# Kernel optimization log

Hardware: AMD Instinct MI355X
Metric: run time of the kernel (lower is better)

The kernel has to match this reference:

```python
import jax, jax.numpy as jnp
import numpy as np

B, D = 128, 64  # batch; channel == height == width == dim == 64 (hardcoded by the module)


def setup_inputs() -> dict:
    key = jax.random.key(0)
    kx, kc, kh, kw = jax.random.split(key, 4)
    x = jax.random.normal(kx, (B, D, D, D), dtype=jnp.float32)
    # Stacked 1x1 conv weights: [i (loop index), out_channels, in_channels]
    Wc = jax.random.normal(kc, (D, D, D), dtype=jnp.float32) * 0.1
    Wh = jax.random.normal(kh, (D, D, D), dtype=jnp.float32) * 0.1
    Ww = jax.random.normal(kw, (D, D, D), dtype=jnp.float32) * 0.1
    return {"x": x, "Wc": Wc, "Wh": Wh, "Ww": Ww}


def reference(x, Wc, Wh, Ww):
    # x: [b, c, h, w] with c == h == w == 64
    # Adaptive avg-pool to 1x1 on three permutations -> three [b, 64] vectors.
    c_vec = x.mean(axis=(2, 3))  # pool over (h, w): channel descriptor   [b, 64]
    h_vec = x.mean(axis=(1, 2))  # pool over (c, h): width descriptor    [b, 64]
    w_vec = x.mean(axis=(1, 3))  # pool over (c, w): height descriptor   [b, 64]

    # All 64 per-iteration 1x1 convs + sigmoid as one batched GEMM per branch.
    # Wc[i, o, j]: weight of the i-th conv; conv(C)[o] = sum_j Wc[i,o,j] * c_vec[b,j]
    fc = jax.nn.sigmoid(jnp.einsum('ioj,bj->bio', Wc, c_vec))  # [b, 64(i), 64]
    fh = jax.nn.sigmoid(jnp.einsum('ioj,bj->bio', Wh, h_vec))  # [b, 64(i), 64]
    fw = jax.nn.sigmoid(jnp.einsum('ioj,bj->bio', Ww, w_vec))  # [b, 64(i), 64]

    # recon: bmm(bmm(C, H), W) == outer product fc_i (x) fh_i (x) fw_i, summed over i.
    LR = jnp.einsum('bic,bip,biq->bcpq', fc, fh, fw)  # [b, 64, 64, 64]
    return LR
```

## Files before the change

### kernel.cpp

```cpp
#include <hip/hip_runtime.h>
#include <hip/hip_bf16.h>


#define NB 128

typedef __attribute__((ext_vector_type(8))) short bf16x8;
typedef __attribute__((ext_vector_type(4))) float f32x4;

__device__ __forceinline__ float bf2f(short s) {
    return __uint_as_float(((unsigned)(unsigned short)s) << 16);
}
__device__ __forceinline__ unsigned packbf2(float a, float b) {
    unsigned ua = __float_as_uint(a); ua += 0x7fffu + ((ua >> 16) & 1u);
    unsigned ub = __float_as_uint(b); ub += 0x7fffu + ((ub >> 16) & 1u);
    return (ua >> 16) | (ub & 0xffff0000u);
}
__device__ __forceinline__ unsigned short f2bf(float f) {
    unsigned u = __float_as_uint(f); u += 0x7fffu + ((u >> 16) & 1u);
    return (unsigned short)(u >> 16);
}

__global__ __launch_bounds__(256) void pool_kernel(const float* __restrict__ x,
                                                   float* __restrict__ cvecT,
                                                   float* __restrict__ hv_part,
                                                   float* __restrict__ wv_part)
{
    const int blk  = blockIdx.x;
    const int b    = blk >> 2;
    const int cblk = blk & 3;
    const int t    = threadIdx.x;
    const int wv   = t >> 6;
    const int l    = t & 63;
    const int lg   = l >> 4;
    const int lw   = l & 15;

    __shared__ float cpart[16][4];
    __shared__ float hsum_l[64];
    __shared__ float wpart[4][64];

    const float* xb = x + (size_t)b * 262144 + (size_t)cblk * 65536;

    float cs[16];
    float acc_h[4] = {0.f, 0.f, 0.f, 0.f};
    float acc_w[4] = {0.f, 0.f, 0.f, 0.f};

#pragma unroll
    for (int cc = 0; cc < 16; ++cc) {
        const float* xc = xb + cc * 4096 + wv * 1024 + 4 * l;
        float sc = 0.f;
#pragma unroll
        for (int k = 0; k < 4; ++k) {
            float4 v = *reinterpret_cast<const float4*>(xc + k * 256);
            float s = (v.x + v.y) + (v.z + v.w);
            sc += s;
            acc_h[k] += s;
            acc_w[0] += v.x; acc_w[1] += v.y; acc_w[2] += v.z; acc_w[3] += v.w;
        }
        cs[cc] = sc;
    }

#pragma unroll
    for (int cc = 0; cc < 16; ++cc) {
        float v = cs[cc];
#pragma unroll
        for (int off = 32; off >= 1; off >>= 1) v += __shfl_xor(v, off, 64);
        if (l == 0) cpart[cc][wv] = v;
    }
#pragma unroll
    for (int k = 0; k < 4; ++k) {
        float v = acc_h[k];
        v += __shfl_xor(v, 1, 64);
        v += __shfl_xor(v, 2, 64);
        v += __shfl_xor(v, 4, 64);
        v += __shfl_xor(v, 8, 64);
        if (lw == 0) hsum_l[wv * 16 + k * 4 + lg] = v;
    }
#pragma unroll
    for (int m = 0; m < 4; ++m) {
        float v = acc_w[m];
        v += __shfl_xor(v, 16, 64);
        v += __shfl_xor(v, 32, 64);
        if (lg == 0) wpart[wv][lw * 4 + m] = v;
    }
    __syncthreads();

    const float scale = 1.f / 4096.f;
    if (t < 16) {
        float s = cpart[t][0] + cpart[t][1] + cpart[t][2] + cpart[t][3];
        cvecT[(cblk * 16 + t) * NB + b] = s * scale;
    }
    if (t < 64) {
        wv_part[(cblk * 64 + t) * NB + b] = hsum_l[t] * scale;
        float ws_ = wpart[0][t] + wpart[1][t] + wpart[2][t] + wpart[3][t];
        hv_part[(cblk * 64 + t) * NB + b] = ws_ * scale;
    }
}

__global__ __launch_bounds__(256) void fvec_kernel(const float* __restrict__ Wc,
                                                   const float* __restrict__ Wh,
                                                   const float* __restrict__ Ww,
                                                   const float* __restrict__ cvecT,
                                                   const float* __restrict__ hv_part,
                                                   const float* __restrict__ wv_part,
                                                   unsigned short* __restrict__ fcT,
                                                   unsigned short* __restrict__ fhT,
                                                   unsigned short* __restrict__ fwT)
{
    const int br = blockIdx.x >> 6;
    const int i  = blockIdx.x & 63;
    const float* W = (br == 0) ? Wc : (br == 1) ? Wh : Ww;
    const float* V = (br == 0) ? cvecT : (br == 1) ? hv_part : wv_part;
    unsigned short* outT = (br == 0) ? fcT : (br == 1) ? fhT : fwT;

    __shared__ float Wt[64][64];
    __shared__ float vl[64 * NB];

    const int t = threadIdx.x;
    {
        const float* Wi = W + (size_t)i * 4096;
#pragma unroll
        for (int r = 0; r < 4; ++r) {
            int f = t + 256 * r;
            float4 v = reinterpret_cast<const float4*>(Wi)[f];
            int o = (4 * f) >> 6;
            int j = (4 * f) & 63;
            Wt[j + 0][o] = v.x; Wt[j + 1][o] = v.y; Wt[j + 2][o] = v.z; Wt[j + 3][o] = v.w;
        }
    }
#pragma unroll
    for (int r = 0; r < 8; ++r) {
        int f = t + 256 * r;
        float4 v = reinterpret_cast<const float4*>(V)[f];
        if (br != 0) {
            float4 v1 = reinterpret_cast<const float4*>(V + 8192)[f];
            float4 v2 = reinterpret_cast<const float4*>(V + 16384)[f];
            float4 v3 = reinterpret_cast<const float4*>(V + 24576)[f];
            v.x += (v1.x + v2.x) + v3.x;
            v.y += (v1.y + v2.y) + v3.y;
            v.z += (v1.z + v2.z) + v3.z;
            v.w += (v1.w + v2.w) + v3.w;
        }
        reinterpret_cast<float4*>(vl)[f] = v;
    }
    __syncthreads();

    const int og = t & 7;
    const int bg = t >> 3;
    const int o0 = og * 8;
    const int b0 = bg * 4;

    float acc[4][8];
#pragma unroll
    for (int bb = 0; bb < 4; ++bb)
#pragma unroll
        for (int oo = 0; oo < 8; ++oo) acc[bb][oo] = 0.f;

#pragma unroll 4
    for (int j = 0; j < 64; ++j) {
        float4 vb = *reinterpret_cast<const float4*>(&vl[j * NB + b0]);
        float4 w0 = *reinterpret_cast<const float4*>(&Wt[j][o0]);
        float4 w1 = *reinterpret_cast<const float4*>(&Wt[j][o0 + 4]);
        float vb_[4] = {vb.x, vb.y, vb.z, vb.w};
        float wv_[8] = {w0.x, w0.y, w0.z, w0.w, w1.x, w1.y, w1.z, w1.w};
#pragma unroll
        for (int bb = 0; bb < 4; ++bb)
#pragma unroll
            for (int oo = 0; oo < 8; ++oo)
                acc[bb][oo] += vb_[bb] * wv_[oo];
    }

#pragma unroll
    for (int bb = 0; bb < 4; ++bb)
#pragma unroll
        for (int oo = 0; oo < 8; ++oo) {
            float sg = 1.f / (1.f + __expf(-acc[bb][oo]));
            outT[((size_t)(b0 + bb) * 64 + (o0 + oo)) * 64 + i] = f2bf(sg);
        }
}

__global__ __launch_bounds__(256) void recon_kernel(const unsigned short* __restrict__ fcT,
                                                    const unsigned short* __restrict__ fhT,
                                                    const unsigned short* __restrict__ fwT,
                                                    float* __restrict__ out)
{
    const int blk  = blockIdx.x;
    const int b    = blk >> 2;
    const int pblk = blk & 3;
    const int t    = threadIdx.x;
    const int w    = t >> 6;
    const int l    = t & 63;
    const int lr   = l & 15;
    const int lg4  = l >> 4;

    __shared__ __align__(16) unsigned short fcl[64 * 72];
    __shared__ __align__(16) unsigned short fwl[64 * 72];
    __shared__ __align__(16) unsigned short fhl[16 * 72];

    const unsigned short* fcb = fcT + (size_t)b * 4096;
    const unsigned short* fwb = fwT + (size_t)b * 4096;
    const unsigned short* fhb = fhT + (size_t)b * 4096 + pblk * 1024;

#pragma unroll
    for (int r = 0; r < 2; ++r) {
        int f = t + 256 * r;
        *reinterpret_cast<int4*>(&fcl[(f >> 3) * 72 + (f & 7) * 8]) =
            reinterpret_cast<const int4*>(fcb)[f];
        *reinterpret_cast<int4*>(&fwl[(f >> 3) * 72 + (f & 7) * 8]) =
            reinterpret_cast<const int4*>(fwb)[f];
    }
    if (t < 128) {
        *reinterpret_cast<int4*>(&fhl[(t >> 3) * 72 + (t & 7) * 8]) =
            reinterpret_cast<const int4*>(fhb)[t];
    }
    __syncthreads();

    bf16x8 afr[4][2], wfr[4][2];
#pragma unroll
    for (int ct = 0; ct < 4; ++ct)
#pragma unroll
        for (int kb = 0; kb < 2; ++kb) {
            afr[ct][kb] = *reinterpret_cast<const bf16x8*>(
                &fcl[(ct * 16 + lr) * 72 + kb * 32 + lg4 * 8]);
            wfr[ct][kb] = *reinterpret_cast<const bf16x8*>(
                &fwl[(ct * 16 + lr) * 72 + kb * 32 + lg4 * 8]);
        }

    for (int pp = 0; pp < 4; ++pp) {
        const int p = w * 4 + pp;
        float hv[16];
#pragma unroll
        for (int kb = 0; kb < 2; ++kb) {
            bf16x8 hf = *reinterpret_cast<const bf16x8*>(
                &fhl[p * 72 + kb * 32 + lg4 * 8]);
#pragma unroll
            for (int j = 0; j < 8; ++j) hv[kb * 8 + j] = bf2f(hf[j]);
        }
#pragma unroll
        for (int qt = 0; qt < 4; ++qt) {
            bf16x8 bfr0, bfr1;
            {
                union { unsigned u[4]; bf16x8 v; } bu;
#pragma unroll
                for (int jj = 0; jj < 4; ++jj) {
                    float p0 = hv[2 * jj]     * bf2f(wfr[qt][0][2 * jj]);
                    float p1 = hv[2 * jj + 1] * bf2f(wfr[qt][0][2 * jj + 1]);
                    bu.u[jj] = packbf2(p0, p1);
                }
                bfr0 = bu.v;
            }
            {
                union { unsigned u[4]; bf16x8 v; } bu;
#pragma unroll
                for (int jj = 0; jj < 4; ++jj) {
                    float p0 = hv[8 + 2 * jj]     * bf2f(wfr[qt][1][2 * jj]);
                    float p1 = hv[8 + 2 * jj + 1] * bf2f(wfr[qt][1][2 * jj + 1]);
                    bu.u[jj] = packbf2(p0, p1);
                }
                bfr1 = bu.v;
            }
#pragma unroll
            for (int ct = 0; ct < 4; ++ct) {
                f32x4 acc = {0.f, 0.f, 0.f, 0.f};
                acc = __builtin_amdgcn_mfma_f32_16x16x32_bf16(afr[ct][0], bfr0, acc, 0, 0, 0);
                acc = __builtin_amdgcn_mfma_f32_16x16x32_bf16(afr[ct][1], bfr1, acc, 0, 0, 0);
                float* ob = out + (((size_t)b * 64 + ct * 16 + lg4 * 4) * 64
                                   + (pblk * 16 + p)) * 64 + qt * 16 + lr;
#pragma unroll
                for (int r = 0; r < 4; ++r) ob[(size_t)r * 4096] = acc[r];
            }
        }
    }
}

extern "C" void kernel_launch(void* const* d_in, const int* in_sizes, int n_in,
                              void* d_out, int out_size, void* d_ws, size_t ws_size,
                              hipStream_t stream) {
    (void)in_sizes; (void)n_in; (void)out_size; (void)ws_size;
    const float* x  = (const float*)d_in[0];
    const float* Wc = (const float*)d_in[1];
    const float* Wh = (const float*)d_in[2];
    const float* Ww = (const float*)d_in[3];
    float* out = (float*)d_out;

    float* ws      = (float*)d_ws;
    float* cvecT   = ws;
    float* hv_part = ws + 8192;
    float* wv_part = ws + 40960;
    unsigned short* fcT = (unsigned short*)(ws + 73728);
    unsigned short* fhT = fcT + 524288;
    unsigned short* fwT = fhT + 524288;

    pool_kernel<<<512, 256, 0, stream>>>(x, cvecT, hv_part, wv_part);
    fvec_kernel<<<192, 256, 0, stream>>>(Wc, Wh, Ww, cvecT, hv_part, wv_part, fcT, fhT, fwT);
    recon_kernel<<<512, 256, 0, stream>>>(fcT, fhT, fwT, out);
}
```

Baseline: 77.66 us.

## Stage recon output through LDS for float4 stores; split pool across 8 blocks

The recon kernel now computes all four q-tiles per channel tile, writes the MFMA accumulators into a per-wave XOR-swizzled LDS bounce buffer, and reads them back as float4 rows. Each row is then stored contiguously, replacing the scattered 4-byte global stores and reducing store transactions on the 128 MB output. Separately, the pooling kernel is split into 8 channel blocks per batch instead of 4, doubling grid parallelism. This costs more partial sums for fvec_kernel to reduce and extra LDS usage in recon.

Result: faster. 70.86 us (-8.8%).

```diff
diff --git a/kernel.cpp b/kernel.cpp
--- a/kernel.cpp
+++ b/kernel.cpp
@@ -26,26 +26,26 @@
                                                    float* __restrict__ wv_part)
 {
     const int blk  = blockIdx.x;
-    const int b    = blk >> 2;
-    const int cblk = blk & 3;
+    const int b    = blk >> 3;
+    const int cblk = blk & 7;
     const int t    = threadIdx.x;
     const int wv   = t >> 6;
     const int l    = t & 63;
     const int lg   = l >> 4;
     const int lw   = l & 15;
 
-    __shared__ float cpart[16][4];
+    __shared__ float cpart[8][4];
     __shared__ float hsum_l[64];
     __shared__ float wpart[4][64];
 
-    const float* xb = x + (size_t)b * 262144 + (size_t)cblk * 65536;
-
-    float cs[16];
+    const float* xb = x + (size_t)b * 262144 + (size_t)cblk * 32768;
+
+    float cs[8];
     float acc_h[4] = {0.f, 0.f, 0.f, 0.f};
     float acc_w[4] = {0.f, 0.f, 0.f, 0.f};
 
 #pragma unroll
-    for (int cc = 0; cc < 16; ++cc) {
+    for (int cc = 0; cc < 8; ++cc) {
         const float* xc = xb + cc * 4096 + wv * 1024 + 4 * l;
         float sc = 0.f;
 #pragma unroll
@@ -60,7 +60,7 @@
     }
 
 #pragma unroll
-    for (int cc = 0; cc < 16; ++cc) {
+    for (int cc = 0; cc < 8; ++cc) {
         float v = cs[cc];
 #pragma unroll
         for (int off = 32; off >= 1; off >>= 1) v += __shfl_xor(v, off, 64);
@@ -85,9 +85,9 @@
     __syncthreads();
 
     const float scale = 1.f / 4096.f;
-    if (t < 16) {
+    if (t < 8) {
         float s = cpart[t][0] + cpart[t][1] + cpart[t][2] + cpart[t][3];
-        cvecT[(cblk * 16 + t) * NB + b] = s * scale;
+        cvecT[(cblk * 8 + t) * NB + b] = s * scale;
     }
     if (t < 64) {
         wv_part[(cblk * 64 + t) * NB + b] = hsum_l[t] * scale;
@@ -132,13 +132,11 @@
         int f = t + 256 * r;
         float4 v = reinterpret_cast<const float4*>(V)[f];
         if (br != 0) {
-            float4 v1 = reinterpret_cast<const float4*>(V + 8192)[f];
-            float4 v2 = reinterpret_cast<const float4*>(V + 16384)[f];
-            float4 v3 = reinterpret_cast<const float4*>(V + 24576)[f];
-            v.x += (v1.x + v2.x) + v3.x;
-            v.y += (v1.y + v2.y) + v3.y;
-            v.z += (v1.z + v2.z) + v3.z;
-            v.w += (v1.w + v2.w) + v3.w;
+#pragma unroll
+            for (int k = 1; k < 8; ++k) {
+                float4 u = reinterpret_cast<const float4*>(V + 8192 * k)[f];
+                v.x += u.x; v.y += u.y; v.z += u.z; v.w += u.w;
+            }
         }
         reinterpret_cast<float4*>(vl)[f] = v;
     }
@@ -195,6 +193,7 @@
     __shared__ __align__(16) unsigned short fcl[64 * 72];
     __shared__ __align__(16) unsigned short fwl[64 * 72];
     __shared__ __align__(16) unsigned short fhl[16 * 72];
+    __shared__ __align__(16) float bounce[4][16 * 72];
 
     const unsigned short* fcb = fcT + (size_t)b * 4096;
     const unsigned short* fwb = fwT + (size_t)b * 4096;
@@ -225,6 +224,8 @@
                 &fwl[(ct * 16 + lr) * 72 + kb * 32 + lg4 * 8]);
         }
 
+    float* bw = &bounce[w][0];
+
     for (int pp = 0; pp < 4; ++pp) {
         const int p = w * 4 + pp;
         float hv[16];
@@ -235,38 +236,44 @@
 #pragma unroll
             for (int j = 0; j < 8; ++j) hv[kb * 8 + j] = bf2f(hf[j]);
         }
+        bf16x8 b0s[4], b1s[4];
 #pragma unroll
         for (int qt = 0; qt < 4; ++qt) {
-            bf16x8 bfr0, bfr1;
-            {
-                union { unsigned u[4]; bf16x8 v; } bu;
-#pragma unroll
-                for (int jj = 0; jj < 4; ++jj) {
-                    float p0 = hv[2 * jj]     * bf2f(wfr[qt][0][2 * jj]);
-                    float p1 = hv[2 * jj + 1] * bf2f(wfr[qt][0][2 * jj + 1]);
-                    bu.u[jj] = packbf2(p0, p1);
-                }
-                bfr0 = bu.v;
+            union { unsigned u[4]; bf16x8 v; } bu0, bu1;
+#pragma unroll
+            for (int jj = 0; jj < 4; ++jj) {
+                float p0 = hv[2 * jj]     * bf2f(wfr[qt][0][2 * jj]);
+                float p1 = hv[2 * jj + 1] * bf2f(wfr[qt][0][2 * jj + 1]);
+                bu0.u[jj] = packbf2(p0, p1);
+                float p2 = hv[8 + 2 * jj]     * bf2f(wfr[qt][1][2 * jj]);
+                float p3 = hv[8 + 2 * jj + 1] * bf2f(wfr[qt][1][2 * jj + 1]);
+                bu1.u[jj] = packbf2(p2, p3);
             }
-            {
-                union { unsigned u[4]; bf16x8 v; } bu;
-#pragma unroll
-                for (int jj = 0; jj < 4; ++jj) {
-                    float p0 = hv[8 + 2 * jj]     * bf2f(wfr[qt][1][2 * jj]);
-                    float p1 = hv[8 + 2 * jj + 1] * bf2f(wfr[qt][1][2 * jj + 1]);
-                    bu.u[jj] = packbf2(p0, p1);
-                }
-                bfr1 = bu.v;
+            b0s[qt] = bu0.v; b1s[qt] = bu1.v;
+        }
+
+#pragma unroll
+        for (int ct = 0; ct < 4; ++ct) {
+            f32x4 acc[4];
+#pragma unroll
+            for (int qt = 0; qt < 4; ++qt) {
+                f32x4 a = {0.f, 0.f, 0.f, 0.f};
+                a = __builtin_amdgcn_mfma_f32_16x16x32_bf16(afr[ct][0], b0s[qt], a, 0, 0, 0);
+                a = __builtin_amdgcn_mfma_f32_16x16x32_bf16(afr[ct][1], b1s[qt], a, 0, 0, 0);
+                acc[qt] = a;
             }
 #pragma unroll
-            for (int ct = 0; ct < 4; ++ct) {
-                f32x4 acc = {0.f, 0.f, 0.f, 0.f};
-                acc = __builtin_amdgcn_mfma_f32_16x16x32_bf16(afr[ct][0], bfr0, acc, 0, 0, 0);
-                acc = __builtin_amdgcn_mfma_f32_16x16x32_bf16(afr[ct][1], bfr1, acc, 0, 0, 0);
-                float* ob = out + (((size_t)b * 64 + ct * 16 + lg4 * 4) * 64
-                                   + (pblk * 16 + p)) * 64 + qt * 16 + lr;
-#pragma unroll
-                for (int r = 0; r < 4; ++r) ob[(size_t)r * 4096] = acc[r];
+            for (int qt = 0; qt < 4; ++qt)
+#pragma unroll
+                for (int r = 0; r < 4; ++r)
+                    bw[(lg4 * 4 + r) * 72 + ((qt * 16 + lr) ^ (lg4 << 4))] = acc[qt][r];
+#pragma unroll
+            for (int i = 0; i < 4; ++i) {
+                int cr = 4 * i + lg4;
+                float4 v = *reinterpret_cast<const float4*>(
+                    &bw[cr * 72 + ((4 * lr) ^ (i << 4))]);
+                *reinterpret_cast<float4*>(
+                    out + (((size_t)b * 64 + ct * 16 + cr) * 64 + pblk * 16 + p) * 64 + 4 * lr) = v;
             }
         }
     }
@@ -285,12 +292,12 @@
     float* ws      = (float*)d_ws;
     float* cvecT   = ws;
     float* hv_part = ws + 8192;
-    float* wv_part = ws + 40960;
-    unsigned short* fcT = (unsigned short*)(ws + 73728);
+    float* wv_part = ws + 73728;
+    unsigned short* fcT = (unsigned short*)(ws + 139264);
     unsigned short* fhT = fcT + 524288;
     unsigned short* fwT = fhT + 524288;
 
-    pool_kernel<<<512, 256, 0, stream>>>(x, cvecT, hv_part, wv_part);
+    pool_kernel<<<1024, 256, 0, stream>>>(x, cvecT, hv_part, wv_part);
     fvec_kernel<<<192, 256, 0, stream>>>(Wc, Wh, Ww, cvecT, hv_part, wv_part, fcT, fhT, fwT);
     recon_kernel<<<512, 256, 0, stream>>>(fcT, fhT, fwT, out);
 }
```
